# Performance work log

Hardware: AMD Instinct MI355X
Metric: run time of the kernel (lower is better)

Reference implementation:

```python
import jax, jax.numpy as jnp
import numpy as np

N = 50000
E = 600000
D_IN = 128
D_HID = 128
D_OUT = 40
BN_EPS = 1e-5


def setup_inputs() -> dict:
    key = jax.random.key(0)
    ks = jax.random.split(key, 16)
    g = lambda k, *s: (jax.random.normal(k, s, jnp.float32) * 0.05)
    return {
        "x": jax.random.normal(ks[0], (N, D_IN), jnp.float32),
        "edge_index": jax.random.randint(ks[1], (2, E), 0, N, dtype=jnp.int64),
        "W0": g(ks[2], D_IN, D_HID), "b0": jnp.zeros((D_HID,), jnp.float32),
        "W1": g(ks[3], D_HID, D_HID), "b1": jnp.zeros((D_HID,), jnp.float32),
        "W2": g(ks[4], D_HID, D_OUT), "b2": jnp.zeros((D_OUT,), jnp.float32),
        "g0": 1.0 + g(ks[5], D_HID), "be0": g(ks[6], D_HID),
        "m0": g(ks[7], D_HID), "v0": 0.5 + jax.random.uniform(ks[8], (D_HID,), jnp.float32),
        "g1": 1.0 + g(ks[9], D_HID), "be1": g(ks[10], D_HID),
        "m1": g(ks[11], D_HID), "v1": 0.5 + jax.random.uniform(ks[12], (D_HID,), jnp.float32),
    }


def reference(x, edge_index, W0, b0, W1, b1, W2, b2,
              g0, be0, m0, v0, g1, be1, m1, v1):
    n = x.shape[0]
    loop = jnp.arange(n, dtype=edge_index.dtype)
    # GCN with self-loops: A_hat = A + I, symmetric normalization
    src = jnp.concatenate([edge_index[0], loop])
    dst = jnp.concatenate([edge_index[1], loop])
    deg = jax.ops.segment_sum(jnp.ones_like(dst, jnp.float32), dst, num_segments=n)
    dinv = jax.lax.rsqrt(jnp.maximum(deg, 1.0))
    norm = dinv[src] * dinv[dst]  # [E+N]

    def conv(h, W, b):
        h = h @ W + b                                   # [N, d_out]
        msg = norm[:, None] * h[src]                    # gather + scale
        return jax.ops.segment_sum(msg, dst, num_segments=n)

    def bn_relu(h, g, be, m, v):
        return jax.nn.relu((h - m) * (g * jax.lax.rsqrt(v + BN_EPS)) + be)

    h = bn_relu(conv(x, W0, b0), g0, be0, m0, v0)
    h = bn_relu(conv(h, W1, b1), g1, be1, m1, v1)
    h = conv(h, W2, b2)
    return jax.nn.log_softmax(h, axis=-1)
```

## Files before the change

### kernel.cpp

```cpp
#include <hip/hip_runtime.h>
#include <math.h>

#define BN_EPS 1e-5f
#define CAP 96

typedef unsigned short ushort_t;
typedef __attribute__((ext_vector_type(8))) short short8;
typedef __attribute__((ext_vector_type(4))) float floatx4;

__device__ inline ushort_t f2b(float f) {
    unsigned u = __float_as_uint(f);
    unsigned r = u + 0x7FFFu + ((u >> 16) & 1u);
    return (ushort_t)(r >> 16);
}
__device__ inline float b2f(ushort_t b) { return __uint_as_float(((unsigned)b) << 16); }
__device__ inline float2 u2f2(unsigned u) {
    return make_float2(b2f((ushort_t)(u & 0xffffu)), b2f((ushort_t)(u >> 16)));
}


__global__ void fill_ell(const int* __restrict__ ei, int* __restrict__ cnt,
                         int* __restrict__ ell, int E) {
    int e = blockIdx.x * blockDim.x + threadIdx.x;
    if (e >= E) return;
    int s = ei[e];
    int d = ei[E + e];
    int p = atomicAdd(&cnt[d], 1);
    if (p < CAP) ell[(size_t)d * CAP + p] = s;
}

__global__ void make_dinv(const int* __restrict__ cnt, float* __restrict__ dinv, int n) {
    int i = blockIdx.x * blockDim.x + threadIdx.x;
    if (i < n) dinv[i] = rsqrtf((float)(cnt[i] + 1));
}

__global__ __launch_bounds__(256) void cast_wt_all(const float* __restrict__ W0,
                                                   const float* __restrict__ W1,
                                                   const float* __restrict__ W2,
                                                   ushort_t* __restrict__ Wt0,
                                                   ushort_t* __restrict__ Wt1,
                                                   ushort_t* __restrict__ Wt2) {
    int i = blockIdx.x * 256 + threadIdx.x;
    if (i < 16384) {
        int n = i >> 7, k = i & 127;
        Wt0[i] = f2b(W0[k * 128 + n]);
    } else if (i < 32768) {
        int j = i - 16384;
        int n = j >> 7, k = j & 127;
        Wt1[j] = f2b(W1[k * 128 + n]);
    } else if (i < 40960) {
        int j = i - 32768;
        int n = j >> 7, k = j & 127;
        Wt2[j] = (n < 40) ? f2b(W2[k * 40 + n]) : (ushort_t)0;
    }
}

template<int NT, bool AF32>
__global__ __launch_bounds__(256) void gemm_mfma(const void* __restrict__ Av,
                                                 const ushort_t* __restrict__ Wt,
                                                 const float* __restrict__ bias,
                                                 const float* __restrict__ dinv,
                                                 ushort_t* __restrict__ C,
                                                 int M, int ncols) {
    __shared__ ushort_t As[128 * 128];
    __shared__ ushort_t Ws[NT * 128];
    const int tid = threadIdx.x;
    const int rbase = blockIdx.x * 128;

#pragma unroll
    for (int p = 0; p < 8; ++p) {
        int cid = p * 256 + tid;
        int gr = rbase + (cid >> 4);
        if (AF32) {
            const float* A32 = (const float*)Av;
            float4 f0 = make_float4(0.f, 0.f, 0.f, 0.f), f1 = f0;
            if (gr < M) {
                f0 = *(const float4*)(A32 + (size_t)rbase * 128 + (size_t)cid * 8);
                f1 = *(const float4*)(A32 + (size_t)rbase * 128 + (size_t)cid * 8 + 4);
            }
            union { ushort_t u[8]; uint4 w; } o;
            o.u[0] = f2b(f0.x); o.u[1] = f2b(f0.y); o.u[2] = f2b(f0.z); o.u[3] = f2b(f0.w);
            o.u[4] = f2b(f1.x); o.u[5] = f2b(f1.y); o.u[6] = f2b(f1.z); o.u[7] = f2b(f1.w);
            *(uint4*)(As + cid * 8) = o.w;
        } else {
            const ushort_t* A16 = (const ushort_t*)Av;
            uint4 val = make_uint4(0, 0, 0, 0);
            if (gr < M) val = *(const uint4*)(A16 + (size_t)rbase * 128 + (size_t)cid * 8);
            *(uint4*)(As + cid * 8) = val;
        }
    }
#pragma unroll
    for (int p = 0; p < NT / 16; ++p) {
        int cid = p * 256 + tid;
        *(uint4*)(Ws + cid * 8) = *(const uint4*)(Wt + (size_t)cid * 8);
    }
    __syncthreads();

    const int wave = tid >> 6, lane = tid & 63;
    const int m = lane & 15, quad = lane >> 4;
    constexpr int CT = NT / 16;
    floatx4 acc[2][CT];
#pragma unroll
    for (int rt = 0; rt < 2; ++rt)
#pragma unroll
        for (int ct = 0; ct < CT; ++ct) acc[rt][ct] = (floatx4){0.f, 0.f, 0.f, 0.f};

    const int r0 = wave * 32;
#pragma unroll
    for (int ks = 0; ks < 4; ++ks) {
        short8 a0 = *(const short8*)(As + (r0 + m) * 128 + ks * 32 + quad * 8);
        short8 a1 = *(const short8*)(As + (r0 + 16 + m) * 128 + ks * 32 + quad * 8);
#pragma unroll
        for (int ct = 0; ct < CT; ++ct) {
            short8 b = *(const short8*)(Ws + (ct * 16 + m) * 128 + ks * 32 + quad * 8);
            acc[0][ct] = __builtin_amdgcn_mfma_f32_16x16x32_bf16(a0, b, acc[0][ct], 0, 0, 0);
            acc[1][ct] = __builtin_amdgcn_mfma_f32_16x16x32_bf16(a1, b, acc[1][ct], 0, 0, 0);
        }
    }

    float dsc[2][4];
#pragma unroll
    for (int rt = 0; rt < 2; ++rt)
#pragma unroll
        for (int r = 0; r < 4; ++r) {
            int gr = rbase + r0 + rt * 16 + quad * 4 + r;
            dsc[rt][r] = (gr < M) ? dinv[gr] : 0.f;
        }

    __syncthreads();
#pragma unroll
    for (int rt = 0; rt < 2; ++rt) {
#pragma unroll
        for (int ct = 0; ct < CT; ++ct) {
            int col = ct * 16 + m;
            float bv = (col < ncols) ? bias[col] : 0.f;
#pragma unroll
            for (int r = 0; r < 4; ++r) {
                int row = r0 + rt * 16 + quad * 4 + r;
                As[row * NT + col] = f2b((acc[rt][ct][r] + bv) * dsc[rt][r]);
            }
        }
    }
    __syncthreads();
    constexpr int CPT = 128 * NT / 8 / 256;
#pragma unroll
    for (int p = 0; p < CPT; ++p) {
        int cid = p * 256 + tid;
        int row = cid / (NT / 8);
        int gr = rbase + row;
        if (gr < M)
            *(uint4*)(C + (size_t)gr * NT + (cid % (NT / 8)) * 8) = *(const uint4*)(As + cid * 8);
    }
}

__global__ __launch_bounds__(256) void agg128_bn(const ushort_t* __restrict__ h,
                                                 const int* __restrict__ cnt,
                                                 const int* __restrict__ ell,
                                                 const float* __restrict__ dinv,
                                                 const float* __restrict__ g,
                                                 const float* __restrict__ be,
                                                 const float* __restrict__ m,
                                                 const float* __restrict__ v,
                                                 ushort_t* __restrict__ out, int n) {
    int wv = __builtin_amdgcn_readfirstlane((blockIdx.x * 256 + threadIdx.x) >> 6);
    int lane = threadIdx.x & 63;
    if (wv >= n) return;
    const unsigned* h2 = (const unsigned*)h;
    float dv = dinv[wv];
    float2 hv = u2f2(h2[(size_t)wv * 64 + lane]);
    float ax = hv.x, ay = hv.y;
    int c = min(cnt[wv], CAP);
    const int* row = ell + (size_t)wv * CAP;
    int k = 0;
    for (; k + 8 <= c; k += 8) {
        int s[8];
#pragma unroll
        for (int j = 0; j < 8; ++j) s[j] = row[k + j];
#pragma unroll
        for (int j = 0; j < 8; ++j) {
            float2 t = u2f2(h2[(size_t)s[j] * 64 + lane]);
            ax += t.x;
            ay += t.y;
        }
    }
    if (k < c) {
        int rem = c - k;
        int s[8];
#pragma unroll
        for (int j = 0; j < 8; ++j) {
            int sr = row[k + j];
            s[j] = (j < rem) ? sr : 0;
        }
#pragma unroll
        for (int j = 0; j < 8; ++j) {
            float2 t = u2f2(h2[(size_t)s[j] * 64 + lane]);
            ax += (j < rem) ? t.x : 0.f;
            ay += (j < rem) ? t.y : 0.f;
        }
    }
    ax *= dv;
    ay *= dv;
    int c0 = lane * 2;
    float s0f = g[c0] * rsqrtf(v[c0] + BN_EPS);
    float s1f = g[c0 + 1] * rsqrtf(v[c0 + 1] + BN_EPS);
    float o0 = fmaxf(fmaf(ax - m[c0], s0f, be[c0]), 0.f);
    float o1 = fmaxf(fmaf(ay - m[c0 + 1], s1f, be[c0 + 1]), 0.f);
    unsigned ov = (unsigned)f2b(o0) | ((unsigned)f2b(o1) << 16);
    ((unsigned*)out)[(size_t)wv * 64 + lane] = ov;
}

__global__ __launch_bounds__(256) void agg40_lsm(const ushort_t* __restrict__ h,
                                                 const int* __restrict__ cnt,
                                                 const int* __restrict__ ell,
                                                 const float* __restrict__ dinv,
                                                 float* __restrict__ out, int n) {
    int wv = __builtin_amdgcn_readfirstlane((blockIdx.x * 256 + threadIdx.x) >> 6);
    int lane = threadIdx.x & 63;
    if (wv >= n) return;
    float dv = dinv[wv];
    float acc = b2f(h[(size_t)wv * 64 + lane]);
    int c = min(cnt[wv], CAP);
    const int* row = ell + (size_t)wv * CAP;
    int k = 0;
    for (; k + 8 <= c; k += 8) {
        int s[8];
#pragma unroll
        for (int j = 0; j < 8; ++j) s[j] = row[k + j];
#pragma unroll
        for (int j = 0; j < 8; ++j) acc += b2f(h[(size_t)s[j] * 64 + lane]);
    }
    if (k < c) {
        int rem = c - k;
        int s[8];
#pragma unroll
        for (int j = 0; j < 8; ++j) {
            int sr = row[k + j];
            s[j] = (j < rem) ? sr : 0;
        }
#pragma unroll
        for (int j = 0; j < 8; ++j) {
            float t = b2f(h[(size_t)s[j] * 64 + lane]);
            acc += (j < rem) ? t : 0.f;
        }
    }
    acc *= dv;
    bool act = lane < 40;
    float x = act ? acc : -INFINITY;
    float mx = x;
#pragma unroll
    for (int off = 32; off > 0; off >>= 1) mx = fmaxf(mx, __shfl_xor(mx, off, 64));
    float ex = act ? expf(acc - mx) : 0.f;
    float se = ex;
#pragma unroll
    for (int off = 32; off > 0; off >>= 1) se += __shfl_xor(se, off, 64);
    float r = acc - mx - logf(se);
    if (act) out[(size_t)wv * 40 + lane] = r;
}


extern "C" void kernel_launch(void* const* d_in, const int* in_sizes, int n_in,
                              void* d_out, int out_size, void* d_ws, size_t ws_size,
                              hipStream_t stream) {
    const float* x = (const float*)d_in[0];
    const int* ei = (const int*)d_in[1];
    const float* W0 = (const float*)d_in[2];
    const float* b0 = (const float*)d_in[3];
    const float* W1 = (const float*)d_in[4];
    const float* b1 = (const float*)d_in[5];
    const float* W2 = (const float*)d_in[6];
    const float* b2 = (const float*)d_in[7];
    const float* g0 = (const float*)d_in[8];
    const float* be0 = (const float*)d_in[9];
    const float* m0 = (const float*)d_in[10];
    const float* v0 = (const float*)d_in[11];
    const float* g1 = (const float*)d_in[12];
    const float* be1 = (const float*)d_in[13];
    const float* m1 = (const float*)d_in[14];
    const float* v1 = (const float*)d_in[15];
    float* out = (float*)d_out;

    const int N = in_sizes[0] / 128;
    const int E = in_sizes[1] / 2;

    char* wp = (char*)d_ws;
    auto alloc = [&](size_t bytes) -> char* {
        char* p = wp;
        wp += (bytes + 255) & ~(size_t)255;
        return p;
    };
    int* cnt = (int*)alloc((size_t)N * 4);
    float* dinv = (float*)alloc((size_t)N * 4);
    int* ell = (int*)alloc(((size_t)N * CAP + 8) * 4);
    ushort_t* hA = (ushort_t*)alloc((size_t)N * 128 * 2);
    ushort_t* hB = (ushort_t*)alloc((size_t)N * 128 * 2);
    ushort_t* hA2 = (ushort_t*)alloc((size_t)N * 128 * 2);
    ushort_t* hB2 = (ushort_t*)alloc((size_t)N * 128 * 2);
    ushort_t* hL = (ushort_t*)alloc((size_t)N * 64 * 2);
    ushort_t* Wt0 = (ushort_t*)alloc(128 * 128 * 2);
    ushort_t* Wt1 = (ushort_t*)alloc(128 * 128 * 2);
    ushort_t* Wt2 = (ushort_t*)alloc(64 * 128 * 2);

    hipMemsetAsync(cnt, 0, (size_t)N * 4, stream);
    fill_ell<<<(E + 255) / 256, 256, 0, stream>>>(ei, cnt, ell, E);
    make_dinv<<<(N + 255) / 256, 256, 0, stream>>>(cnt, dinv, N);
    cast_wt_all<<<160, 256, 0, stream>>>(W0, W1, W2, Wt0, Wt1, Wt2);

    int gblocks = (N + 127) / 128;
    gemm_mfma<128, true><<<gblocks, 256, 0, stream>>>(x, Wt0, b0, dinv, hA, N, 128);
    agg128_bn<<<(N + 3) / 4, 256, 0, stream>>>(hA, cnt, ell, dinv, g0, be0, m0, v0, hB, N);
    gemm_mfma<128, false><<<gblocks, 256, 0, stream>>>(hB, Wt1, b1, dinv, hA2, N, 128);
    agg128_bn<<<(N + 3) / 4, 256, 0, stream>>>(hA2, cnt, ell, dinv, g1, be1, m1, v1, hB2, N);
    gemm_mfma<64, false><<<gblocks, 256, 0, stream>>>(hB2, Wt2, b2, dinv, hL, N, 40);
    agg40_lsm<<<(N + 3) / 4, 256, 0, stream>>>(hL, cnt, ell, dinv, out, N);
}
```

Measured before the change: 240.8 us.

## Split 128-wide aggregation into column slices across 4 nodes per wave; merge prep kernels

```diff
diff --git a/kernel.cpp b/kernel.cpp
--- a/kernel.cpp
+++ b/kernel.cpp
@@ -29,29 +29,29 @@
     if (p < CAP) ell[(size_t)d * CAP + p] = s;
 }
 
-__global__ void make_dinv(const int* __restrict__ cnt, float* __restrict__ dinv, int n) {
-    int i = blockIdx.x * blockDim.x + threadIdx.x;
-    if (i < n) dinv[i] = rsqrtf((float)(cnt[i] + 1));
-}
-
-__global__ __launch_bounds__(256) void cast_wt_all(const float* __restrict__ W0,
-                                                   const float* __restrict__ W1,
-                                                   const float* __restrict__ W2,
-                                                   ushort_t* __restrict__ Wt0,
-                                                   ushort_t* __restrict__ Wt1,
-                                                   ushort_t* __restrict__ Wt2) {
+__global__ __launch_bounds__(256) void prep(const float* __restrict__ W0,
+                                            const float* __restrict__ W1,
+                                            const float* __restrict__ W2,
+                                            ushort_t* __restrict__ Wt0,
+                                            ushort_t* __restrict__ Wt1,
+                                            ushort_t* __restrict__ Wt2,
+                                            const int* __restrict__ cnt,
+                                            float* __restrict__ dinv, int n) {
     int i = blockIdx.x * 256 + threadIdx.x;
     if (i < 16384) {
-        int n = i >> 7, k = i & 127;
-        Wt0[i] = f2b(W0[k * 128 + n]);
+        int c = i >> 7, k = i & 127;
+        Wt0[i] = f2b(W0[k * 128 + c]);
     } else if (i < 32768) {
         int j = i - 16384;
-        int n = j >> 7, k = j & 127;
-        Wt1[j] = f2b(W1[k * 128 + n]);
+        int c = j >> 7, k = j & 127;
+        Wt1[j] = f2b(W1[k * 128 + c]);
     } else if (i < 40960) {
         int j = i - 32768;
-        int n = j >> 7, k = j & 127;
-        Wt2[j] = (n < 40) ? f2b(W2[k * 40 + n]) : (ushort_t)0;
+        int c = j >> 7, k = j & 127;
+        Wt2[j] = (c < 40) ? f2b(W2[k * 40 + c]) : (ushort_t)0;
+    } else {
+        int j = i - 40960;
+        if (j < n) dinv[j] = rsqrtf((float)(cnt[j] + 1));
     }
 }
 
@@ -162,15 +162,20 @@
                                                  const float* __restrict__ m,
                                                  const float* __restrict__ v,
                                                  ushort_t* __restrict__ out, int n) {
-    int wv = __builtin_amdgcn_readfirstlane((blockIdx.x * 256 + threadIdx.x) >> 6);
-    int lane = threadIdx.x & 63;
-    if (wv >= n) return;
+    const int tid = threadIdx.x;
+    const int lane = tid & 63;
+    const int grp = lane >> 4;
+    const int ci = lane & 15;
+    const int wvb = blockIdx.x * 4 + (tid >> 6);
+    const int node = wvb * 4 + grp;
+    const int colu = blockIdx.y * 16 + ci;
+    if (node >= n) return;
     const unsigned* h2 = (const unsigned*)h;
-    float dv = dinv[wv];
-    float2 hv = u2f2(h2[(size_t)wv * 64 + lane]);
+    float dv = dinv[node];
+    float2 hv = u2f2(h2[(size_t)node * 64 + colu]);
     float ax = hv.x, ay = hv.y;
-    int c = min(cnt[wv], CAP);
-    const int* row = ell + (size_t)wv * CAP;
+    int c = min(cnt[node], CAP);
+    const int* row = ell + (size_t)node * CAP;
     int k = 0;
     for (; k + 8 <= c; k += 8) {
         int s[8];
@@ -178,7 +183,7 @@
         for (int j = 0; j < 8; ++j) s[j] = row[k + j];
 #pragma unroll
         for (int j = 0; j < 8; ++j) {
-            float2 t = u2f2(h2[(size_t)s[j] * 64 + lane]);
+            float2 t = u2f2(h2[(size_t)s[j] * 64 + colu]);
             ax += t.x;
             ay += t.y;
         }
@@ -193,20 +198,20 @@
         }
 #pragma unroll
         for (int j = 0; j < 8; ++j) {
-            float2 t = u2f2(h2[(size_t)s[j] * 64 + lane]);
+            float2 t = u2f2(h2[(size_t)s[j] * 64 + colu]);
             ax += (j < rem) ? t.x : 0.f;
             ay += (j < rem) ? t.y : 0.f;
         }
     }
     ax *= dv;
     ay *= dv;
-    int c0 = lane * 2;
+    int c0 = colu * 2;
     float s0f = g[c0] * rsqrtf(v[c0] + BN_EPS);
     float s1f = g[c0 + 1] * rsqrtf(v[c0 + 1] + BN_EPS);
     float o0 = fmaxf(fmaf(ax - m[c0], s0f, be[c0]), 0.f);
     float o1 = fmaxf(fmaf(ay - m[c0 + 1], s1f, be[c0 + 1]), 0.f);
     unsigned ov = (unsigned)f2b(o0) | ((unsigned)f2b(o1) << 16);
-    ((unsigned*)out)[(size_t)wv * 64 + lane] = ov;
+    ((unsigned*)out)[(size_t)node * 64 + colu] = ov;
 }
 
 __global__ __launch_bounds__(256) void agg40_lsm(const ushort_t* __restrict__ h,
@@ -302,14 +307,14 @@
 
     hipMemsetAsync(cnt, 0, (size_t)N * 4, stream);
     fill_ell<<<(E + 255) / 256, 256, 0, stream>>>(ei, cnt, ell, E);
-    make_dinv<<<(N + 255) / 256, 256, 0, stream>>>(cnt, dinv, N);
-    cast_wt_all<<<160, 256, 0, stream>>>(W0, W1, W2, Wt0, Wt1, Wt2);
+    prep<<<(40960 + N + 255) / 256, 256, 0, stream>>>(W0, W1, W2, Wt0, Wt1, Wt2, cnt, dinv, N);
 
     int gblocks = (N + 127) / 128;
+    dim3 agrid((N + 15) / 16, 4);
     gemm_mfma<128, true><<<gblocks, 256, 0, stream>>>(x, Wt0, b0, dinv, hA, N, 128);
-    agg128_bn<<<(N + 3) / 4, 256, 0, stream>>>(hA, cnt, ell, dinv, g0, be0, m0, v0, hB, N);
+    agg128_bn<<<agrid, 256, 0, stream>>>(hA, cnt, ell, dinv, g0, be0, m0, v0, hB, N);
     gemm_mfma<128, false><<<gblocks, 256, 0, stream>>>(hB, Wt1, b1, dinv, hA2, N, 128);
-    agg128_bn<<<(N + 3) / 4, 256, 0, stream>>>(hA2, cnt, ell, dinv, g1, be1, m1, v1, hB2, N);
+    agg128_bn<<<agrid, 256, 0, stream>>>(hA2, cnt, ell, dinv, g1, be1, m1, v1, hB2, N);
     gemm_mfma<64, false><<<gblocks, 256, 0, stream>>>(hB2, Wt2, b2, dinv, hL, N, 40);
     agg40_lsm<<<(N + 3) / 4, 256, 0, stream>>>(hL, cnt, ell, dinv, out, N);
 }
```

Result: slower. 260.5 us (+8.2%).

## Store ELL neighbor indices as 16-bit, pad rows with a zero sentinel node

Applied to the files above, without the earlier changes.

```diff
diff --git a/kernel.cpp b/kernel.cpp
--- a/kernel.cpp
+++ b/kernel.cpp
@@ -20,38 +20,57 @@
 
 
 __global__ void fill_ell(const int* __restrict__ ei, int* __restrict__ cnt,
-                         int* __restrict__ ell, int E) {
+                         ushort_t* __restrict__ ell, int E) {
     int e = blockIdx.x * blockDim.x + threadIdx.x;
     if (e >= E) return;
     int s = ei[e];
     int d = ei[E + e];
     int p = atomicAdd(&cnt[d], 1);
-    if (p < CAP) ell[(size_t)d * CAP + p] = s;
-}
-
-__global__ void make_dinv(const int* __restrict__ cnt, float* __restrict__ dinv, int n) {
-    int i = blockIdx.x * blockDim.x + threadIdx.x;
-    if (i < n) dinv[i] = rsqrtf((float)(cnt[i] + 1));
-}
-
-__global__ __launch_bounds__(256) void cast_wt_all(const float* __restrict__ W0,
-                                                   const float* __restrict__ W1,
-                                                   const float* __restrict__ W2,
-                                                   ushort_t* __restrict__ Wt0,
-                                                   ushort_t* __restrict__ Wt1,
-                                                   ushort_t* __restrict__ Wt2) {
+    if (p < CAP) ell[(size_t)d * CAP + p] = (ushort_t)s;
+}
+
+__global__ __launch_bounds__(256) void prep(const float* __restrict__ W0,
+                                            const float* __restrict__ W1,
+                                            const float* __restrict__ W2,
+                                            ushort_t* __restrict__ Wt0,
+                                            ushort_t* __restrict__ Wt1,
+                                            ushort_t* __restrict__ Wt2,
+                                            const int* __restrict__ cnt,
+                                            float* __restrict__ dinv,
+                                            ushort_t* __restrict__ ell,
+                                            ushort_t* __restrict__ hA,
+                                            ushort_t* __restrict__ hB,
+                                            ushort_t* __restrict__ hA2,
+                                            ushort_t* __restrict__ hB2,
+                                            ushort_t* __restrict__ hL,
+                                            int n) {
     int i = blockIdx.x * 256 + threadIdx.x;
     if (i < 16384) {
-        int n = i >> 7, k = i & 127;
-        Wt0[i] = f2b(W0[k * 128 + n]);
+        int c = i >> 7, k = i & 127;
+        Wt0[i] = f2b(W0[k * 128 + c]);
     } else if (i < 32768) {
         int j = i - 16384;
-        int n = j >> 7, k = j & 127;
-        Wt1[j] = f2b(W1[k * 128 + n]);
+        int c = j >> 7, k = j & 127;
+        Wt1[j] = f2b(W1[k * 128 + c]);
     } else if (i < 40960) {
         int j = i - 32768;
-        int n = j >> 7, k = j & 127;
-        Wt2[j] = (n < 40) ? f2b(W2[k * 40 + n]) : (ushort_t)0;
+        int c = j >> 7, k = j & 127;
+        Wt2[j] = (c < 40) ? f2b(W2[k * 40 + c]) : (ushort_t)0;
+    } else if (i < 40960 + n) {
+        int j = i - 40960;
+        int c = cnt[j];
+        dinv[j] = rsqrtf((float)(c + 1));
+        c = min(c, CAP);
+        int cp = (c + 7) & ~7;
+        ushort_t* row = ell + (size_t)j * CAP;
+        for (int p = c; p < cp; ++p) row[p] = (ushort_t)n;
+    } else {
+        int t = i - 40960 - n;
+        if (t < 128) hA[(size_t)n * 128 + t] = 0;
+        else if (t < 256) hB[(size_t)n * 128 + (t - 128)] = 0;
+        else if (t < 384) hA2[(size_t)n * 128 + (t - 256)] = 0;
+        else if (t < 512) hB2[(size_t)n * 128 + (t - 384)] = 0;
+        else if (t < 576) hL[(size_t)n * 64 + (t - 512)] = 0;
     }
 }
 
@@ -155,7 +174,7 @@
 
 __global__ __launch_bounds__(256) void agg128_bn(const ushort_t* __restrict__ h,
                                                  const int* __restrict__ cnt,
-                                                 const int* __restrict__ ell,
+                                                 const ushort_t* __restrict__ ell,
                                                  const float* __restrict__ dinv,
                                                  const float* __restrict__ g,
                                                  const float* __restrict__ be,
@@ -169,10 +188,9 @@
     float dv = dinv[wv];
     float2 hv = u2f2(h2[(size_t)wv * 64 + lane]);
     float ax = hv.x, ay = hv.y;
-    int c = min(cnt[wv], CAP);
-    const int* row = ell + (size_t)wv * CAP;
-    int k = 0;
-    for (; k + 8 <= c; k += 8) {
+    int cp = (min(cnt[wv], CAP) + 7) & ~7;
+    const ushort_t* row = ell + (size_t)wv * CAP;
+    for (int k = 0; k < cp; k += 8) {
         int s[8];
 #pragma unroll
         for (int j = 0; j < 8; ++j) s[j] = row[k + j];
@@ -181,21 +199,6 @@
             float2 t = u2f2(h2[(size_t)s[j] * 64 + lane]);
             ax += t.x;
             ay += t.y;
-        }
-    }
-    if (k < c) {
-        int rem = c - k;
-        int s[8];
-#pragma unroll
-        for (int j = 0; j < 8; ++j) {
-            int sr = row[k + j];
-            s[j] = (j < rem) ? sr : 0;
-        }
-#pragma unroll
-        for (int j = 0; j < 8; ++j) {
-            float2 t = u2f2(h2[(size_t)s[j] * 64 + lane]);
-            ax += (j < rem) ? t.x : 0.f;
-            ay += (j < rem) ? t.y : 0.f;
         }
     }
     ax *= dv;
@@ -211,7 +214,7 @@
 
 __global__ __launch_bounds__(256) void agg40_lsm(const ushort_t* __restrict__ h,
                                                  const int* __restrict__ cnt,
-                                                 const int* __restrict__ ell,
+                                                 const ushort_t* __restrict__ ell,
                                                  const float* __restrict__ dinv,
                                                  float* __restrict__ out, int n) {
     int wv = __builtin_amdgcn_readfirstlane((blockIdx.x * 256 + threadIdx.x) >> 6);
@@ -219,29 +222,14 @@
     if (wv >= n) return;
     float dv = dinv[wv];
     float acc = b2f(h[(size_t)wv * 64 + lane]);
-    int c = min(cnt[wv], CAP);
-    const int* row = ell + (size_t)wv * CAP;
-    int k = 0;
-    for (; k + 8 <= c; k += 8) {
+    int cp = (min(cnt[wv], CAP) + 7) & ~7;
+    const ushort_t* row = ell + (size_t)wv * CAP;
+    for (int k = 0; k < cp; k += 8) {
         int s[8];
 #pragma unroll
         for (int j = 0; j < 8; ++j) s[j] = row[k + j];
 #pragma unroll
         for (int j = 0; j < 8; ++j) acc += b2f(h[(size_t)s[j] * 64 + lane]);
-    }
-    if (k < c) {
-        int rem = c - k;
-        int s[8];
-#pragma unroll
-        for (int j = 0; j < 8; ++j) {
-            int sr = row[k + j];
-            s[j] = (j < rem) ? sr : 0;
-        }
-#pragma unroll
-        for (int j = 0; j < 8; ++j) {
-            float t = b2f(h[(size_t)s[j] * 64 + lane]);
-            acc += (j < rem) ? t : 0.f;
-        }
     }
     acc *= dv;
     bool act = lane < 40;
@@ -290,20 +278,20 @@
     };
     int* cnt = (int*)alloc((size_t)N * 4);
     float* dinv = (float*)alloc((size_t)N * 4);
-    int* ell = (int*)alloc(((size_t)N * CAP + 8) * 4);
-    ushort_t* hA = (ushort_t*)alloc((size_t)N * 128 * 2);
-    ushort_t* hB = (ushort_t*)alloc((size_t)N * 128 * 2);
-    ushort_t* hA2 = (ushort_t*)alloc((size_t)N * 128 * 2);
-    ushort_t* hB2 = (ushort_t*)alloc((size_t)N * 128 * 2);
-    ushort_t* hL = (ushort_t*)alloc((size_t)N * 64 * 2);
+    ushort_t* ell = (ushort_t*)alloc(((size_t)N * CAP + 16) * 2);
+    ushort_t* hA = (ushort_t*)alloc((size_t)(N + 1) * 128 * 2);
+    ushort_t* hB = (ushort_t*)alloc((size_t)(N + 1) * 128 * 2);
+    ushort_t* hA2 = (ushort_t*)alloc((size_t)(N + 1) * 128 * 2);
+    ushort_t* hB2 = (ushort_t*)alloc((size_t)(N + 1) * 128 * 2);
+    ushort_t* hL = (ushort_t*)alloc((size_t)(N + 1) * 64 * 2);
     ushort_t* Wt0 = (ushort_t*)alloc(128 * 128 * 2);
     ushort_t* Wt1 = (ushort_t*)alloc(128 * 128 * 2);
     ushort_t* Wt2 = (ushort_t*)alloc(64 * 128 * 2);
 
     hipMemsetAsync(cnt, 0, (size_t)N * 4, stream);
     fill_ell<<<(E + 255) / 256, 256, 0, stream>>>(ei, cnt, ell, E);
-    make_dinv<<<(N + 255) / 256, 256, 0, stream>>>(cnt, dinv, N);
-    cast_wt_all<<<160, 256, 0, stream>>>(W0, W1, W2, Wt0, Wt1, Wt2);
+    prep<<<(40960 + N + 576 + 255) / 256, 256, 0, stream>>>(
+        W0, W1, W2, Wt0, Wt1, Wt2, cnt, dinv, ell, hA, hB, hA2, hB2, hL, N);
 
     int gblocks = (N + 127) / 128;
     gemm_mfma<128, true><<<gblocks, 256, 0, stream>>>(x, Wt0, b0, dinv, hA, N, 128);
```

After: 241.7 us. No clear change (+0.4%).
